# Kernel tuning notes

Hardware: AMD Instinct MI355X
Metric: run time of the kernel (lower is better)

Reference implementation:

```python
import jax, jax.numpy as jnp
import numpy as np

V, D, N, K, T, S = 128000, 128, 4, 4, 16, 5
EPS = 1e-10


def setup_inputs() -> dict:
    key = jax.random.key(0)
    k = jax.random.split(key, 5)
    return {
        "E": jax.random.normal(k[0], (V, D), jnp.float32) * 0.02,
        "bases": jax.random.normal(k[1], (K, N, D, D), jnp.float32) * (1.5 / np.sqrt(D)),
        "tension": jax.random.normal(k[2], (K, N, N), jnp.float32) * 0.1,
        "temperature": jnp.ones((K,), jnp.float32),
        "target_sim": jnp.full((K,), -1.0 / (N - 1), jnp.float32),
        "step_size": jnp.full((K,), 0.1, jnp.float32),
        "gate_logit": jnp.full((K,), -2.0, jnp.float32),
        "decay_base": jnp.asarray(0.8, jnp.float32),
        "sensitivity": jnp.asarray(1.0, jnp.float32),
        "noise": jax.random.normal(k[3], (T, K, S, N, D), jnp.float32),
        "tokens": jax.random.randint(k[4], (T,), 0, V),
    }


def reference(E, bases, tension, temperature, target_sim, step_size, gate_logit,
              decay_base, sensitivity, noise, tokens):
    mask = 1.0 - jnp.eye(N, dtype=E.dtype)
    temp = jnp.clip(jnp.abs(temperature), 0.01, None)
    # gauge interaction weights per foam: softmax over bubbles, self-interaction masked
    interaction = jax.nn.softmax(-tension / temp[:, None, None], axis=-1) * mask  # [K,N,N]
    step = jnp.clip(jnp.abs(step_size), 0.001, 0.5)           # [K]
    gate = jax.nn.sigmoid(gate_logit)                          # [K] noise gate
    sens = jnp.abs(sensitivity)

    def equilibrate(state0, B, inter, tgt, stp, g, nz):
        # state0 [N,D]; B [N,D,D] per-bubble bases; nz [S,N,D] pre-drawn perturbations
        def body(state, eps):
            expr = jnp.einsum('nd,nkd->nk', state, B)          # state_i @ basis_i.T
            expr_n = expr / (jnp.linalg.norm(expr, axis=-1, keepdims=True) + EPS)
            cos = expr_n @ expr_n.T                            # [N,N] pairwise cos-sim
            fmag = (cos - tgt) * inter                         # [N,N] force magnitudes
            diff = expr[:, None, :] - expr[None, :, :]         # [N,N,D]
            diff_n = diff / (jnp.linalg.norm(diff, axis=-1, keepdims=True) + EPS)
            f_shared = (fmag[..., None] * diff_n).sum(axis=1)  # [N,D]
            f_local = jnp.einsum('nk,nkd->nd', f_shared, B)    # back to local gauge
            scale = jnp.linalg.norm(state, axis=-1).mean() + EPS
            return state + stp * f_local + g * eps * scale * 0.01, None
        state, _ = jax.lax.scan(body, state0, nz)
        return state

    def foam_step(x, memory, B, inter, tgt, stp, g, nz):
        # x [D]; memory [N,D]
        mem_mean = memory.mean(axis=0)
        mem_norm = jnp.linalg.norm(mem_mean) + EPS
        x_norm = jnp.linalg.norm(x) + EPS
        nov = 1.0 - (x * mem_mean).sum() / (x_norm * mem_norm)
        novelty = jnp.where(mem_norm > 1e-8, nov, 1.0)
        decay = jax.nn.sigmoid(decay_base - sens * novelty)
        xm = x + decay * mem_mean
        eq = equilibrate(jnp.broadcast_to(xm, (N, D)), B, inter, tgt, stp, g, nz)
        rho = (eq.T @ eq) / ((eq * eq).sum() + EPS)            # trace-normalized density
        mem_new = decay * memory + (1.0 - decay) * eq
        return rho, mem_new

    xs_tok = E[tokens]                                         # [T,D]

    def token_step(memories, inp):
        x, nz_t = inp
        rhos, memories = jax.vmap(foam_step, in_axes=(None, 0, 0, 0, 0, 0, 0, 0))(
            x, memories, bases, interaction, target_sim, step, gate, nz_t)
        rho_mix = rhos.mean(axis=0)                            # [D,D]
        eig = jnp.clip(jnp.linalg.eigvalsh(rho_mix), 1e-12, None)
        eig = eig / eig.sum()
        logits = ((E @ rho_mix) * E).sum(axis=-1)              # born rule [V]
        logp = jax.nn.log_softmax(logits)
        probs = jnp.exp(logp)
        S_rho = -(eig * jnp.clip(jnp.log(eig), -100.0, None)).sum()
        H_tok = -(probs * jnp.clip(logp, -100.0, None)).sum()
        return memories, (probs, S_rho, H_tok, H_tok - S_rho)

    mem0 = jnp.zeros((K, N, D), E.dtype)
    _, (probs, S_rho, H_tok, F_tok) = jax.lax.scan(token_step, mem0, (xs_tok, noise))
    return probs, S_rho, H_tok, F_tok
```

## Files before the change

kernel.cpp:

```cpp
#include <hip/hip_runtime.h>
#include <math.h>

#define V_ 128000
#define D_ 128
#define N_ 4
#define K_ 4
#define T_ 16
#define S_ 5
#define EPSF 1e-10f

#define WS_G      0
#define WS_BEPS   262144
#define WS_BX     917504
#define WS_EQ2    950272
#define WS_EQBALL 954368
#define WS_GRAM   970752
#define WS_MM     974848
#define WS_BMM    975360
#define WS_INTER  977408
#define WS_WK     977472
#define WS_SRHO   977728
#define WS_LNZ    977744
#define WS_ZPART  977760
#define WS_EQF    977760
#define WS_HPART  1009760

typedef __attribute__((ext_vector_type(8))) short short8v;
typedef __attribute__((ext_vector_type(4))) float float4v;

__device__ __forceinline__ short bfb(float x) {
    unsigned u = __float_as_uint(x);
    u += 0x7fffu + ((u >> 16) & 1u);
    return (short)(u >> 16);
}

__device__ __forceinline__ void jpair(int x, int r, int& ox, bool& isp) {
    if (x == 15) { ox = r % 15; isp = true; return; }
    int s = x - r; s %= 15; if (s < 0) s += 15;
    if (s == 0) { ox = 15; isp = false; return; }
    int o = 2 * r - x; o %= 15; if (o < 0) o += 15;
    ox = o;
    isp = (s <= 7);
}

__device__ __forceinline__ void rotfast(float app, float aqq, float apq, float& c, float& s) {
    c = 1.f; s = 0.f;
    if (fabsf(apq) > 1e-20f) {
        float tau = (aqq - app) * 0.5f * __builtin_amdgcn_rcpf(apq);
        float sq1 = __builtin_amdgcn_sqrtf(1.f + tau * tau);
        float den = tau + ((tau >= 0.f) ? sq1 : -sq1);
        float tt = __builtin_amdgcn_rcpf(den);
        c = __builtin_amdgcn_rsqf(1.f + tt * tt);
        s = tt * c;
    }
}

__global__ __launch_bounds__(256)
void i2_prep(const float* __restrict__ bases, const float* __restrict__ E,
             const float* __restrict__ noise, const int* __restrict__ tokens,
             const float* __restrict__ tension, const float* __restrict__ temperature,
             float* __restrict__ ws)
{
    int tid = threadIdx.x;
    if (blockIdx.x == 64) {
        if (tid < 4) {
            int k = tid;
            float temp = fmaxf(fabsf(temperature[k]), 0.01f);
            for (int i = 0; i < 4; ++i) {
                float v[4]; float mx = -1e30f;
                for (int j = 0; j < 4; ++j) { v[j] = -tension[k*16 + i*4 + j] / temp; mx = fmaxf(mx, v[j]); }
                float se = 0.f;
                for (int j = 0; j < 4; ++j) { v[j] = expf(v[j] - mx); se += v[j]; }
                for (int j = 0; j < 4; ++j) ws[WS_INTER + k*16 + i*4 + j] = (i == j) ? 0.0f : v[j] / se;
            }
        }
        return;
    }
    int kn = blockIdx.x >> 2, q = blockIdx.x & 3;
    int k = kn >> 2, n = kn & 3;
    __shared__ __align__(16) float Blds[128 * 132];
    const float4* B4 = (const float4*)(bases + (size_t)kn * 16384);
    for (int idx = tid; idx < 4096; idx += 256) {
        int jrow = idx >> 5, c = idx & 31;
        float4 v = B4[jrow * 32 + c];
        *((float4*)&Blds[jrow * 132 + c * 4]) = v;
    }
    __syncthreads();
    int j1 = q * 32 + (tid >> 3);
    int l = tid & 7;
    float accg[16];
#pragma unroll
    for (int i = 0; i < 16; ++i) accg[i] = 0.f;
    for (int c = 0; c < 32; ++c) {
        float4 b1 = *((const float4*)&Blds[j1 * 132 + c * 4]);
#pragma unroll
        for (int i = 0; i < 16; ++i) {
            float4 b2 = *((const float4*)&Blds[(l + 8 * i) * 132 + c * 4]);
            accg[i] += b1.x * b2.x + b1.y * b2.y + b1.z * b2.z + b1.w * b2.w;
        }
    }
#pragma unroll
    for (int i = 0; i < 16; ++i) {
        int j2 = l + 8 * i;
        ws[WS_G + (((size_t)kn * 32 + (j2 >> 2)) * 128 + j1) * 4 + (j2 & 3)] = accg[i];
    }
    __shared__ __align__(16) float vecl[128];
    __shared__ float vred[2][128];
    int jv = tid & 127, ch = tid >> 7;
    for (int vi = q * 24; vi < q * 24 + 24; ++vi) {
        const float* src; int dstoff;
        if (vi < 16) {
            int tt = vi;
            src = E + (size_t)tokens[tt] * 128;
            dstoff = WS_BX + (tt * 4 + k) * 512 + n * 128;
        } else {
            int r2 = vi - 16; int tt = r2 / 5, s2 = r2 % 5;
            size_t off = (size_t)(((tt * 4 + k) * 5 + s2) * 4 + n) * 128;
            src = noise + off;
            dstoff = WS_BEPS + (int)off;
        }
        if (tid < 32) ((float4*)vecl)[tid] = ((const float4*)src)[tid];
        __syncthreads();
        float a2 = 0.f;
        for (int c = ch * 16; c < ch * 16 + 16; ++c) {
            float4 bv = *((const float4*)&Blds[jv * 132 + c * 4]);
            float4 xv = ((const float4*)vecl)[c];
            a2 += bv.x * xv.x + bv.y * xv.y + bv.z * xv.z + bv.w * xv.w;
        }
        vred[ch][jv] = a2;
        __syncthreads();
        if (tid < 128) ws[dstoff + tid] = vred[0][tid] + vred[1][tid];
        __syncthreads();
    }
}

__global__ __launch_bounds__(512, 2)
void kap_all(const float* __restrict__ E, const float* __restrict__ noise,
             const int* __restrict__ tokens, const float* __restrict__ bases,
             const float* __restrict__ target_sim, const float* __restrict__ step_size,
             const float* __restrict__ gate_logit, const float* __restrict__ decay_base,
             const float* __restrict__ sensitivity, float* __restrict__ ws)
{
    const int k = blockIdx.x;
    const int tid = threadIdx.x;
    const int n = tid >> 7;
    const int d = tid & 127;
    const int lane = tid & 63;
    const int wh = (tid >> 6) & 1;
    const int kn = k * 4 + n;

    __shared__ float xl[128];
    __shared__ __align__(16) float mlL[128];
    __shared__ __align__(16) float aL[4][128], exL[4][128];
    __shared__ float bmmL[4][128];
    __shared__ float interL[16];
    __shared__ float wredL[4][2][8];
    __shared__ float wredC[4][8];
    __shared__ float scal[1];

    float4 g[32];
    const float4* G4 = (const float4*)(ws + WS_G);
#pragma unroll
    for (int c = 0; c < 32; ++c) g[c] = G4[((size_t)kn * 32 + c) * 128 + d];

    if (tid < 16) interL[tid] = ws[WS_INTER + k * 16 + tid];
    if (tid < 128) mlL[tid] = 0.f;
    bmmL[n][d] = 0.f;

    const float tgt = target_sim[k];
    const float stp = fminf(fmaxf(fabsf(step_size[k]), 0.001f), 0.5f);
    const float gate = 1.0f / (1.0f + expf(-gate_logit[k]));
    const float dbase = decay_base[0];
    const float sens = fabsf(sensitivity[0]);
    __syncthreads();

#pragma unroll 1
    for (int t = 0; t < T_; ++t) {
        int tok = tokens[t];
        if (tid < 128) xl[tid] = E[(size_t)tok * 128 + tid];
        __syncthreads();

        if (tid < 64) {
            float x0 = xl[tid], x1 = xl[tid + 64];
            float m0 = mlL[tid], m1 = mlL[tid + 64];
            float vx = x0*x0 + x1*x1, vm = m0*m0 + m1*m1, vd = x0*m0 + x1*m1;
            for (int m = 32; m; m >>= 1) { vx += __shfl_xor(vx, m); vm += __shfl_xor(vm, m); vd += __shfl_xor(vd, m); }
            if (tid == 0) {
                float xnorm = sqrtf(vx) + EPSF, mnorm = sqrtf(vm) + EPSF;
                float nov = 1.0f - vd / (xnorm * mnorm);
                float novelty = (mnorm > 1e-8f) ? nov : 1.0f;
                scal[0] = 1.0f / (1.0f + expf(-(dbase - sens * novelty)));
            }
        }
        __syncthreads();
        const float dec = scal[0];

        float e0 = ws[WS_BX + (t*4 + k)*512 + n*128 + d] + dec * bmmL[n][d];
        float u  = xl[d] + dec * mlL[d];
        float ex = e0, a = 0.f, be = 0.f;
        exL[n][d] = ex;
        __syncthreads();

        for (int s = 0; s < 5; ++s) {
            int nz = (((t*4 + k)*5 + s)*4 + n) * 128 + d;
            float bepsv = ws[WS_BEPS + nz];
            float noisev = noise[nz];
            float em[4];
#pragma unroll
            for (int m = 0; m < 4; ++m) em[m] = exL[m][d];
            float r[7];
#pragma unroll
            for (int m = 0; m < 4; ++m) r[m] = ex * em[m];
            r[4] = u * u;
            r[5] = (e0 + be) * a;
            r[6] = a * (ex - e0 - be);
#pragma unroll
            for (int m2 = 32; m2; m2 >>= 1) {
#pragma unroll
                for (int q = 0; q < 7; ++q) r[q] += __shfl_xor(r[q], m2);
            }
            if (lane == 0) {
#pragma unroll
                for (int q = 0; q < 7; ++q) wredL[n][wh][q] = r[q];
            }
            __syncthreads();
            if (tid < 32) {
                int nn = tid >> 3, q = tid & 7;
                if (q < 7) wredC[nn][q] = wredL[nn][0][q] + wredL[nn][1][q];
            }
            __syncthreads();
            float ssum = 0.f;
#pragma unroll
            for (int m = 0; m < 4; ++m)
                ssum += sqrtf(fmaxf(wredC[m][4] + 2.f*wredC[m][5] + wredC[m][6], 0.f));
            float cn = gate * (0.25f * ssum + EPSF) * 0.01f;

            float Pnn = wredC[n][n];
            float enn = sqrtf(fmaxf(Pnn, 0.f)) + EPSF;
            float fsh = 0.f;
#pragma unroll
            for (int m = 0; m < 4; ++m) {
                float Pmm = wredC[m][m];
                float Pnm = wredC[n][m];
                float enm = sqrtf(fmaxf(Pmm, 0.f)) + EPSF;
                float cosnm = Pnm / (enn * enm);
                float fm = (cosnm - tgt) * interL[n * 4 + m];
                float dnn = sqrtf(fmaxf(Pnn - 2.f*Pnm + Pmm, 0.f)) + EPSF;
                float w = fm / dnn;
                fsh += w * (ex - em[m]);
            }
            a += stp * fsh;
            be += cn * bepsv;
            u += cn * noisev;
            aL[n][d] = a;
            __syncthreads();
            const float4* a4 = (const float4*)aL[n];
            float y = 0.f;
#pragma unroll
            for (int c = 0; c < 32; ++c) {
                float4 av = a4[c];
                y += g[c].x*av.x + g[c].y*av.y + g[c].z*av.z + g[c].w*av.w;
            }
            ex = e0 + y + be;
            exL[n][d] = ex;
            __syncthreads();
        }

        {
            const float* Bp = bases + (size_t)kn * 16384;
            float acc = 0.f;
#pragma unroll 8
            for (int j = 0; j < 128; ++j) acc += aL[n][j] * Bp[(size_t)j * 128 + d];
            float eq = u + acc;
            ws[WS_EQF + ((size_t)t * 16 + kn) * 128 + d] = eq;
            unsigned short* eqb = (unsigned short*)(ws + WS_EQBALL);
            int c2 = d >> 5, lg = (d >> 3) & 3, j8 = d & 7;
            eqb[t*2048 + (c2*64 + lg*16 + kn)*8 + j8] = (unsigned short)bfb(eq);
            float sq = eq * eq;
            for (int m = 32; m; m >>= 1) sq += __shfl_xor(sq, m);
            if (lane == 0) wredL[n][wh][7] = sq;
            exL[n][d] = eq;
            __syncthreads();
            if (tid < 4) {
                float s4 = 0.f;
#pragma unroll
                for (int m = 0; m < 4; ++m) s4 += wredL[m][0][7] + wredL[m][1][7];
                ws[WS_WK + t*16 + 4*k + tid] = 1.0f / (4.0f * (s4 + EPSF));
            }
            if (tid < 128) {
                float eqm = 0.25f * (exL[0][tid] + exL[1][tid] + exL[2][tid] + exL[3][tid]);
                mlL[tid] = dec * mlL[tid] + (1.f - dec) * eqm;
            }
            __syncthreads();
            const float4* Br = (const float4*)(bases + (size_t)kn * 16384 + (size_t)d * 128);
            const float4* mm4 = (const float4*)mlL;
            float bacc = 0.f;
#pragma unroll 8
            for (int c = 0; c < 32; ++c) {
                float4 bv = Br[c], mv = mm4[c];
                bacc += bv.x*mv.x + bv.y*mv.y + bv.z*mv.z + bv.w*mv.w;
            }
            bmmL[n][d] = bacc;
            __syncthreads();
        }
    }
}

__global__ __launch_bounds__(256)
void gramk(float* __restrict__ ws)
{
    int t = blockIdx.x, tid = threadIdx.x;
    int i = tid >> 4, j = tid & 15;
    const float4* ra = (const float4*)(ws + WS_EQF + ((size_t)t * 16 + i) * 128);
    const float4* rb = (const float4*)(ws + WS_EQF + ((size_t)t * 16 + j) * 128);
    float dp = 0.f;
#pragma unroll 8
    for (int c = 0; c < 32; ++c) {
        float4 a = ra[c], b2 = rb[c];
        dp += a.x * b2.x + a.y * b2.y + a.z * b2.z + a.w * b2.w;
    }
    ws[WS_GRAM + t * 256 + tid] = dp;
}

__global__ __launch_bounds__(256, 2)
void mega(const float* __restrict__ E, float* __restrict__ ws, float* __restrict__ out)
{
    int b = blockIdx.x, tid = threadIdx.x;
    if (b < 16) {
        if (tid >= 64) return;
        int tt = b;
        __shared__ float Am[16 * 20];
        __shared__ float cR[16], sR[16];
        int i0 = tid >> 2, j40 = (tid & 3) * 4;
        const float* G = ws + WS_GRAM + tt * 256;
        float wv4[4];
#pragma unroll
        for (int kk = 0; kk < 4; ++kk) {
            float ss = G[(4*kk+0)*17] + G[(4*kk+1)*17] + G[(4*kk+2)*17] + G[(4*kk+3)*17];
            wv4[kk] = 1.0f / (4.0f * (ss + EPSF));
        }
#pragma unroll
        for (int m = 0; m < 4; ++m) {
            int jjv = j40 + m;
            Am[i0 * 20 + jjv] = sqrtf(wv4[i0 >> 2] * wv4[jjv >> 2]) * G[i0 * 16 + jjv];
        }
        for (int sw = 0; sw < 6; ++sw) {
            for (int r = 0; r < 15; ++r) {
                if (tid < 8) {
                    int p, q;
                    if (tid == 0) { p = 15; q = r % 15; }
                    else { p = (r + tid) % 15; q = (r - tid + 15) % 15; }
                    float c, s;
                    rotfast(Am[p * 20 + p], Am[q * 20 + q], Am[p * 20 + q], c, s);
                    cR[p] = c; sR[p] = -s;
                    cR[q] = c; sR[q] = s;
                }
                int oi; bool ip; jpair(i0, r, oi, ip);
                float ci = cR[i0], siS = sR[i0];
                float nv[4];
#pragma unroll
                for (int m = 0; m < 4; ++m) {
                    int jjv = j40 + m;
                    int oj; bool jp2; jpair(jjv, r, oj, jp2);
                    float cj = cR[jjv], sjS = sR[jjv];
                    float a00 = Am[i0 * 20 + jjv], a01 = Am[i0 * 20 + oj];
                    float a10 = Am[oi * 20 + jjv], a11 = Am[oi * 20 + oj];
                    nv[m] = ci*cj*a00 + ci*sjS*a01 + siS*cj*a10 + siS*sjS*a11;
                }
#pragma unroll
                for (int m = 0; m < 4; ++m) Am[i0 * 20 + j40 + m] = nv[m];
            }
        }
        if (tid == 0) {
            float tot = 112.0f * 1e-12f;
            float lc[16];
            for (int a2 = 0; a2 < 16; ++a2) { lc[a2] = fmaxf(Am[a2 * 20 + a2], 1e-12f); tot += lc[a2]; }
            float S = 0.f;
            for (int a2 = 0; a2 < 16; ++a2) { float pp = lc[a2] / tot; S -= pp * fmaxf(logf(pp), -100.f); }
            float p0 = 1e-12f / tot;
            S -= 112.f * p0 * fmaxf(logf(p0), -100.f);
            out[(size_t)T_ * V_ + tt] = S;
            ws[WS_SRHO + tt] = S;
        }
        return;
    }
    int b2 = b - 16;
    int pass = b2 / 500;
    int bb = b2 - pass * 500;
    int tok0 = pass * 4;
    int lane = tid & 63, wv = tid >> 6;
    const short8v* eqB = (const short8v*)(ws + WS_EQBALL);
    short8v bfr[4][4];
#pragma unroll
    for (int tk = 0; tk < 4; ++tk)
#pragma unroll
        for (int c2 = 0; c2 < 4; ++c2) bfr[tk][c2] = eqB[(tok0 + tk) * 256 + c2 * 64 + lane];
    float wk[4], zl[4];
#pragma unroll
    for (int tk = 0; tk < 4; ++tk) {
        wk[tk] = ws[WS_WK + (tok0 + tk) * 16 + (lane & 15)];
        zl[tk] = 0.f;
    }
    int tilebase = (bb * 4 + wv) * 64;
#pragma unroll
    for (int it = 0; it < 4; ++it) {
        int rowB = tilebase + it * 16;
        const float* Erow = E + (size_t)(rowB + (lane & 15)) * 128 + ((lane >> 4) * 8);
        float4v acc[4];
#pragma unroll
        for (int tk = 0; tk < 4; ++tk) acc[tk] = (float4v){0.f, 0.f, 0.f, 0.f};
#pragma unroll
        for (int c2 = 0; c2 < 4; ++c2) {
            float4 e0 = *((const float4*)(Erow + c2 * 32));
            float4 e1 = *((const float4*)(Erow + c2 * 32 + 4));
            short8v a;
            a[0] = bfb(e0.x); a[1] = bfb(e0.y); a[2] = bfb(e0.z); a[3] = bfb(e0.w);
            a[4] = bfb(e1.x); a[5] = bfb(e1.y); a[6] = bfb(e1.z); a[7] = bfb(e1.w);
#pragma unroll
            for (int tk = 0; tk < 4; ++tk)
                acc[tk] = __builtin_amdgcn_mfma_f32_16x16x32_bf16(a, bfr[tk][c2], acc[tk], 0, 0, 0);
        }
#pragma unroll
        for (int tk = 0; tk < 4; ++tk) {
            float l0 = wk[tk] * acc[tk][0] * acc[tk][0];
            float l1 = wk[tk] * acc[tk][1] * acc[tk][1];
            float l2 = wk[tk] * acc[tk][2] * acc[tk][2];
            float l3 = wk[tk] * acc[tk][3] * acc[tk][3];
#pragma unroll
            for (int m = 1; m <= 8; m <<= 1) {
                l0 += __shfl_xor(l0, m); l1 += __shfl_xor(l1, m);
                l2 += __shfl_xor(l2, m); l3 += __shfl_xor(l3, m);
            }
            if ((lane & 15) == 0) {
                float4 st; st.x = l0; st.y = l1; st.z = l2; st.w = l3;
                *((float4*)(out + (size_t)(tok0 + tk) * V_ + rowB + (lane >> 4) * 4)) = st;
                zl[tk] += __expf(l0) + __expf(l1) + __expf(l2) + __expf(l3);
            }
        }
    }
#pragma unroll
    for (int tk = 0; tk < 4; ++tk) {
        float z = zl[tk];
        z += __shfl_xor(z, 16); z += __shfl_xor(z, 32);
        if (lane == 0) ws[WS_ZPART + (tok0 + tk) * 2000 + bb * 4 + wv] = z;
    }
}

__global__ __launch_bounds__(256)
void zk(float* __restrict__ ws)
{
    int b = blockIdx.x, tid = threadIdx.x;
    double s = 0.0;
    for (int i = tid; i < 2000; i += 256) s += (double)ws[WS_ZPART + b * 2000 + i];
    for (int m = 32; m; m >>= 1) s += __shfl_xor(s, m);
    __shared__ double sr[4];
    if ((tid & 63) == 0) sr[tid >> 6] = s;
    __syncthreads();
    if (tid == 0) ws[WS_LNZ + b] = (float)log(sr[0] + sr[1] + sr[2] + sr[3]);
}

__global__ __launch_bounds__(256)
void fin1(float* __restrict__ ws, float* __restrict__ out)
{
    int b = blockIdx.x, tid = threadIdx.x;
    int tt = b / 125, blk = b - tt * 125;
    int v = blk * 1024 + tid * 4;
    float lnZ = ws[WS_LNZ + tt];
    float* po = out + (size_t)tt * V_ + v;
    float4 l4 = *((const float4*)po);
    float lp0 = l4.x - lnZ, lp1 = l4.y - lnZ, lp2 = l4.z - lnZ, lp3 = l4.w - lnZ;
    float p0 = __expf(lp0), p1 = __expf(lp1), p2 = __expf(lp2), p3 = __expf(lp3);
    float4 st; st.x = p0; st.y = p1; st.z = p2; st.w = p3;
    *((float4*)po) = st;
    float hp = p0 * fmaxf(lp0, -100.f) + p1 * fmaxf(lp1, -100.f)
             + p2 * fmaxf(lp2, -100.f) + p3 * fmaxf(lp3, -100.f);
    for (int m = 32; m; m >>= 1) hp += __shfl_xor(hp, m);
    __shared__ float hr[4];
    if ((tid & 63) == 0) hr[tid >> 6] = hp;
    __syncthreads();
    if (tid == 0) ws[WS_HPART + tt * 125 + blk] = hr[0] + hr[1] + hr[2] + hr[3];
}

__global__ __launch_bounds__(128)
void f2_final(float* __restrict__ ws, float* __restrict__ out)
{
    int t = blockIdx.x, tid = threadIdx.x;
    float s = (tid < 125) ? ws[WS_HPART + t * 125 + tid] : 0.f;
    for (int m = 32; m; m >>= 1) s += __shfl_xor(s, m);
    __shared__ float sr[2];
    if ((tid & 63) == 0) sr[tid >> 6] = s;
    __syncthreads();
    if (tid == 0) {
        float H = -(sr[0] + sr[1]);
        float S = ws[WS_SRHO + t];
        out[(size_t)T_ * V_ + T_ + t] = H;
        out[(size_t)T_ * V_ + 2 * T_ + t] = H - S;
    }
}

extern "C" void kernel_launch(void* const* d_in, const int* in_sizes, int n_in,
                              void* d_out, int out_size, void* d_ws, size_t ws_size,
                              hipStream_t stream)
{
    (void)in_sizes; (void)n_in; (void)out_size; (void)ws_size;
    const float* E           = (const float*)d_in[0];
    const float* bases       = (const float*)d_in[1];
    const float* tension     = (const float*)d_in[2];
    const float* temperature = (const float*)d_in[3];
    const float* target_sim  = (const float*)d_in[4];
    const float* step_size   = (const float*)d_in[5];
    const float* gate_logit  = (const float*)d_in[6];
    const float* decay_base  = (const float*)d_in[7];
    const float* sensitivity = (const float*)d_in[8];
    const float* noise       = (const float*)d_in[9];
    const int*   tokens      = (const int*)d_in[10];
    float* out = (float*)d_out;
    float* ws  = (float*)d_ws;

    i2_prep<<<65, 256, 0, stream>>>(bases, E, noise, tokens, tension, temperature, ws);
    kap_all<<<4, 512, 0, stream>>>(E, noise, tokens, bases, target_sim, step_size,
                                   gate_logit, decay_base, sensitivity, ws);
    gramk<<<16, 256, 0, stream>>>(ws);
    mega<<<2016, 256, 0, stream>>>(E, ws, out);
    zk<<<16, 256, 0, stream>>>(ws);
    fin1<<<T_ * 125, 256, 0, stream>>>(ws, out);
    f2_final<<<T_, 128, 0, stream>>>(ws, out);
}
```

Measured before the change: 646.2 us.

## Shrink recurrence kernel to one wave per bubble, fuse gram, widen logits tile

The sequential recurrence kernel now runs 256 threads with each wave owning one bubble and two dims per lane. This lets reductions finish within a wave, removes a cross-wave LDS stage and several barriers per step, and prefetches noise, tokens and memory projections into registers. The separate gram kernel is folded into the mega kernel's first blocks, reusing the freed noise-projection buffer for the equilibrium output. The logits GEMM now processes 8 tokens per block instead of 4, halving E reads at the cost of more registers.

```diff
diff --git a/kernel.cpp b/kernel.cpp
--- a/kernel.cpp
+++ b/kernel.cpp
@@ -12,17 +12,12 @@
 #define WS_G      0
 #define WS_BEPS   262144
 #define WS_BX     917504
-#define WS_EQ2    950272
 #define WS_EQBALL 954368
-#define WS_GRAM   970752
-#define WS_MM     974848
-#define WS_BMM    975360
 #define WS_INTER  977408
 #define WS_WK     977472
 #define WS_SRHO   977728
 #define WS_LNZ    977744
 #define WS_ZPART  977760
-#define WS_EQF    977760
 #define WS_HPART  1009760
 
 typedef __attribute__((ext_vector_type(8))) short short8v;
@@ -134,7 +129,7 @@
     }
 }
 
-__global__ __launch_bounds__(512, 2)
+__global__ __launch_bounds__(256, 1)
 void kap_all(const float* __restrict__ E, const float* __restrict__ noise,
              const int* __restrict__ tokens, const float* __restrict__ bases,
              const float* __restrict__ target_sim, const float* __restrict__ step_size,
@@ -143,183 +138,172 @@
 {
     const int k = blockIdx.x;
     const int tid = threadIdx.x;
-    const int n = tid >> 7;
-    const int d = tid & 127;
+    const int n = tid >> 6;
     const int lane = tid & 63;
-    const int wh = (tid >> 6) & 1;
+    const int d0 = lane, d1 = lane + 64;
     const int kn = k * 4 + n;
 
     __shared__ float xl[128];
     __shared__ __align__(16) float mlL[128];
     __shared__ __align__(16) float aL[4][128], exL[4][128];
-    __shared__ float bmmL[4][128];
     __shared__ float interL[16];
-    __shared__ float wredL[4][2][8];
-    __shared__ float wredC[4][8];
-    __shared__ float scal[1];
-
-    float4 g[32];
+    __shared__ float diagP[4], sP[4], sq7[4];
+
+    float4 g0[32], g1[32];
     const float4* G4 = (const float4*)(ws + WS_G);
 #pragma unroll
-    for (int c = 0; c < 32; ++c) g[c] = G4[((size_t)kn * 32 + c) * 128 + d];
+    for (int c = 0; c < 32; ++c) {
+        g0[c] = G4[((size_t)kn * 32 + c) * 128 + d0];
+        g1[c] = G4[((size_t)kn * 32 + c) * 128 + d1];
+    }
 
     if (tid < 16) interL[tid] = ws[WS_INTER + k * 16 + tid];
     if (tid < 128) mlL[tid] = 0.f;
-    bmmL[n][d] = 0.f;
 
     const float tgt = target_sim[k];
     const float stp = fminf(fmaxf(fabsf(step_size[k]), 0.001f), 0.5f);
     const float gate = 1.0f / (1.0f + expf(-gate_logit[k]));
     const float dbase = decay_base[0];
     const float sens = fabsf(sensitivity[0]);
+
+    float xr = (tid < 128) ? E[(size_t)tokens[0] * 128 + tid] : 0.f;
+    float bmm0 = 0.f, bmm1 = 0.f;
     __syncthreads();
+    float w_inter[4];
+#pragma unroll
+    for (int m = 0; m < 4; ++m) w_inter[m] = interL[n * 4 + m];
 
 #pragma unroll 1
     for (int t = 0; t < T_; ++t) {
-        int tok = tokens[t];
-        if (tid < 128) xl[tid] = E[(size_t)tok * 128 + tid];
+        if (tid < 128) xl[tid] = xr;
         __syncthreads();
-
-        if (tid < 64) {
-            float x0 = xl[tid], x1 = xl[tid + 64];
-            float m0 = mlL[tid], m1 = mlL[tid + 64];
-            float vx = x0*x0 + x1*x1, vm = m0*m0 + m1*m1, vd = x0*m0 + x1*m1;
-            for (int m = 32; m; m >>= 1) { vx += __shfl_xor(vx, m); vm += __shfl_xor(vm, m); vd += __shfl_xor(vd, m); }
-            if (tid == 0) {
-                float xnorm = sqrtf(vx) + EPSF, mnorm = sqrtf(vm) + EPSF;
-                float nov = 1.0f - vd / (xnorm * mnorm);
-                float novelty = (mnorm > 1e-8f) ? nov : 1.0f;
-                scal[0] = 1.0f / (1.0f + expf(-(dbase - sens * novelty)));
-            }
-        }
+        if (t + 1 < T_ && tid < 128) xr = E[(size_t)tokens[t + 1] * 128 + tid];
+
+        float bep0[5], bep1[5], no0[5], no1[5];
+#pragma unroll
+        for (int s = 0; s < 5; ++s) {
+            int nz = (((t * 4 + k) * 5 + s) * 4 + n) * 128;
+            bep0[s] = ws[WS_BEPS + nz + d0]; bep1[s] = ws[WS_BEPS + nz + d1];
+            no0[s] = noise[nz + d0];         no1[s] = noise[nz + d1];
+        }
+        float bx0 = ws[WS_BX + (t * 4 + k) * 512 + n * 128 + d0];
+        float bx1 = ws[WS_BX + (t * 4 + k) * 512 + n * 128 + d1];
+
+        float x0 = xl[d0], x1 = xl[d1], m0 = mlL[d0], m1 = mlL[d1];
+        float vx = x0 * x0 + x1 * x1, vm = m0 * m0 + m1 * m1, vd = x0 * m0 + x1 * m1;
+        for (int m = 32; m; m >>= 1) { vx += __shfl_xor(vx, m); vm += __shfl_xor(vm, m); vd += __shfl_xor(vd, m); }
+        float xnorm = sqrtf(vx) + EPSF, mnorm = sqrtf(vm) + EPSF;
+        float nov = 1.0f - vd / (xnorm * mnorm);
+        float novelty = (mnorm > 1e-8f) ? nov : 1.0f;
+        const float dec = 1.0f / (1.0f + expf(-(dbase - sens * novelty)));
+
+        float e00 = bx0 + dec * bmm0, e01 = bx1 + dec * bmm1;
+        float u0 = x0 + dec * m0, u1 = x1 + dec * m1;
+        float ex0 = e00, ex1 = e01, a0 = 0.f, a1 = 0.f, be0 = 0.f, be1 = 0.f;
+        exL[n][d0] = ex0; exL[n][d1] = ex1;
         __syncthreads();
-        const float dec = scal[0];
-
-        float e0 = ws[WS_BX + (t*4 + k)*512 + n*128 + d] + dec * bmmL[n][d];
-        float u  = xl[d] + dec * mlL[d];
-        float ex = e0, a = 0.f, be = 0.f;
-        exL[n][d] = ex;
-        __syncthreads();
 
         for (int s = 0; s < 5; ++s) {
-            int nz = (((t*4 + k)*5 + s)*4 + n) * 128 + d;
-            float bepsv = ws[WS_BEPS + nz];
-            float noisev = noise[nz];
-            float em[4];
-#pragma unroll
-            for (int m = 0; m < 4; ++m) em[m] = exL[m][d];
+            float em0[4], em1[4];
+#pragma unroll
+            for (int m = 0; m < 4; ++m) { em0[m] = exL[m][d0]; em1[m] = exL[m][d1]; }
             float r[7];
 #pragma unroll
-            for (int m = 0; m < 4; ++m) r[m] = ex * em[m];
-            r[4] = u * u;
-            r[5] = (e0 + be) * a;
-            r[6] = a * (ex - e0 - be);
+            for (int m = 0; m < 4; ++m) r[m] = ex0 * em0[m] + ex1 * em1[m];
+            r[4] = u0 * u0 + u1 * u1;
+            r[5] = (e00 + be0) * a0 + (e01 + be1) * a1;
+            r[6] = a0 * (ex0 - e00 - be0) + a1 * (ex1 - e01 - be1);
 #pragma unroll
             for (int m2 = 32; m2; m2 >>= 1) {
 #pragma unroll
                 for (int q = 0; q < 7; ++q) r[q] += __shfl_xor(r[q], m2);
             }
-            if (lane == 0) {
-#pragma unroll
-                for (int q = 0; q < 7; ++q) wredL[n][wh][q] = r[q];
-            }
+            float sn = sqrtf(fmaxf(r[4] + 2.f * r[5] + r[6], 0.f));
+            if (lane == 0) { diagP[n] = r[n]; sP[n] = sn; }
             __syncthreads();
-            if (tid < 32) {
-                int nn = tid >> 3, q = tid & 7;
-                if (q < 7) wredC[nn][q] = wredL[nn][0][q] + wredL[nn][1][q];
-            }
-            __syncthreads();
-            float ssum = 0.f;
-#pragma unroll
-            for (int m = 0; m < 4; ++m)
-                ssum += sqrtf(fmaxf(wredC[m][4] + 2.f*wredC[m][5] + wredC[m][6], 0.f));
+            float ssum = ((sP[0] + sP[1]) + sP[2]) + sP[3];
             float cn = gate * (0.25f * ssum + EPSF) * 0.01f;
 
-            float Pnn = wredC[n][n];
+            float Pnn = r[n];
             float enn = sqrtf(fmaxf(Pnn, 0.f)) + EPSF;
-            float fsh = 0.f;
+            float fsh0 = 0.f, fsh1 = 0.f;
 #pragma unroll
             for (int m = 0; m < 4; ++m) {
-                float Pmm = wredC[m][m];
-                float Pnm = wredC[n][m];
+                float Pmm = diagP[m];
+                float Pnm = r[m];
                 float enm = sqrtf(fmaxf(Pmm, 0.f)) + EPSF;
                 float cosnm = Pnm / (enn * enm);
-                float fm = (cosnm - tgt) * interL[n * 4 + m];
-                float dnn = sqrtf(fmaxf(Pnn - 2.f*Pnm + Pmm, 0.f)) + EPSF;
+                float fm = (cosnm - tgt) * w_inter[m];
+                float dnn = sqrtf(fmaxf(Pnn - 2.f * Pnm + Pmm, 0.f)) + EPSF;
                 float w = fm / dnn;
-                fsh += w * (ex - em[m]);
-            }
-            a += stp * fsh;
-            be += cn * bepsv;
-            u += cn * noisev;
-            aL[n][d] = a;
-            __syncthreads();
+                fsh0 += w * (ex0 - em0[m]);
+                fsh1 += w * (ex1 - em1[m]);
+            }
+            a0 += stp * fsh0; a1 += stp * fsh1;
+            be0 += cn * bep0[s]; be1 += cn * bep1[s];
+            u0 += cn * no0[s];   u1 += cn * no1[s];
+            aL[n][d0] = a0; aL[n][d1] = a1;
             const float4* a4 = (const float4*)aL[n];
-            float y = 0.f;
+            float y0 = 0.f, y1 = 0.f;
 #pragma unroll
             for (int c = 0; c < 32; ++c) {
                 float4 av = a4[c];
-                y += g[c].x*av.x + g[c].y*av.y + g[c].z*av.z + g[c].w*av.w;
-            }
-            ex = e0 + y + be;
-            exL[n][d] = ex;
+                y0 += g0[c].x * av.x + g0[c].y * av.y + g0[c].z * av.z + g0[c].w * av.w;
+                y1 += g1[c].x * av.x + g1[c].y * av.y + g1[c].z * av.z + g1[c].w * av.w;
+            }
+            ex0 = e00 + y0 + be0; ex1 = e01 + y1 + be1;
+            exL[n][d0] = ex0; exL[n][d1] = ex1;
             __syncthreads();
         }
 
         {
             const float* Bp = bases + (size_t)kn * 16384;
-            float acc = 0.f;
+            float acc0 = 0.f, acc1 = 0.f;
 #pragma unroll 8
-            for (int j = 0; j < 128; ++j) acc += aL[n][j] * Bp[(size_t)j * 128 + d];
-            float eq = u + acc;
-            ws[WS_EQF + ((size_t)t * 16 + kn) * 128 + d] = eq;
+            for (int j = 0; j < 128; ++j) {
+                float aj = aL[n][j];
+                acc0 += aj * Bp[(size_t)j * 128 + d0];
+                acc1 += aj * Bp[(size_t)j * 128 + d1];
+            }
+            float eq0 = u0 + acc0, eq1 = u1 + acc1;
+            int eqfbase = WS_BEPS + t * 10240 + k * 2560 + n * 128;
+            ws[eqfbase + d0] = eq0; ws[eqfbase + d1] = eq1;
             unsigned short* eqb = (unsigned short*)(ws + WS_EQBALL);
-            int c2 = d >> 5, lg = (d >> 3) & 3, j8 = d & 7;
-            eqb[t*2048 + (c2*64 + lg*16 + kn)*8 + j8] = (unsigned short)bfb(eq);
-            float sq = eq * eq;
+            {
+                int c2 = d0 >> 5, lg = (d0 >> 3) & 3, j8 = d0 & 7;
+                eqb[t * 2048 + (c2 * 64 + lg * 16 + kn) * 8 + j8] = (unsigned short)bfb(eq0);
+            }
+            {
+                int c2 = d1 >> 5, lg = (d1 >> 3) & 3, j8 = d1 & 7;
+                eqb[t * 2048 + (c2 * 64 + lg * 16 + kn) * 8 + j8] = (unsigned short)bfb(eq1);
+            }
+            float sq = eq0 * eq0 + eq1 * eq1;
             for (int m = 32; m; m >>= 1) sq += __shfl_xor(sq, m);
-            if (lane == 0) wredL[n][wh][7] = sq;
-            exL[n][d] = eq;
+            if (lane == 0) sq7[n] = sq;
+            exL[n][d0] = eq0; exL[n][d1] = eq1;
             __syncthreads();
             if (tid < 4) {
-                float s4 = 0.f;
-#pragma unroll
-                for (int m = 0; m < 4; ++m) s4 += wredL[m][0][7] + wredL[m][1][7];
-                ws[WS_WK + t*16 + 4*k + tid] = 1.0f / (4.0f * (s4 + EPSF));
+                float s4 = sq7[0] + sq7[1] + sq7[2] + sq7[3];
+                ws[WS_WK + t * 16 + 4 * k + tid] = 1.0f / (4.0f * (s4 + EPSF));
             }
             if (tid < 128) {
                 float eqm = 0.25f * (exL[0][tid] + exL[1][tid] + exL[2][tid] + exL[3][tid]);
                 mlL[tid] = dec * mlL[tid] + (1.f - dec) * eqm;
             }
             __syncthreads();
-            const float4* Br = (const float4*)(bases + (size_t)kn * 16384 + (size_t)d * 128);
+            const float4* Br0 = (const float4*)(bases + (size_t)kn * 16384 + (size_t)d0 * 128);
+            const float4* Br1 = (const float4*)(bases + (size_t)kn * 16384 + (size_t)d1 * 128);
             const float4* mm4 = (const float4*)mlL;
-            float bacc = 0.f;
+            bmm0 = 0.f; bmm1 = 0.f;
 #pragma unroll 8
             for (int c = 0; c < 32; ++c) {
-                float4 bv = Br[c], mv = mm4[c];
-                bacc += bv.x*mv.x + bv.y*mv.y + bv.z*mv.z + bv.w*mv.w;
-            }
-            bmmL[n][d] = bacc;
-            __syncthreads();
-        }
-    }
-}
-
-__global__ __launch_bounds__(256)
-void gramk(float* __restrict__ ws)
-{
-    int t = blockIdx.x, tid = threadIdx.x;
-    int i = tid >> 4, j = tid & 15;
-    const float4* ra = (const float4*)(ws + WS_EQF + ((size_t)t * 16 + i) * 128);
-    const float4* rb = (const float4*)(ws + WS_EQF + ((size_t)t * 16 + j) * 128);
-    float dp = 0.f;
-#pragma unroll 8
-    for (int c = 0; c < 32; ++c) {
-        float4 a = ra[c], b2 = rb[c];
-        dp += a.x * b2.x + a.y * b2.y + a.z * b2.z + a.w * b2.w;
-    }
-    ws[WS_GRAM + t * 256 + tid] = dp;
+                float4 mv = mm4[c];
+                float4 v0 = Br0[c], v1 = Br1[c];
+                bmm0 += v0.x * mv.x + v0.y * mv.y + v0.z * mv.z + v0.w * mv.w;
+                bmm1 += v1.x * mv.x + v1.y * mv.y + v1.z * mv.z + v1.w * mv.w;
+            }
+        }
+    }
 }
 
 __global__ __launch_bounds__(256, 2)
@@ -327,12 +311,26 @@
 {
     int b = blockIdx.x, tid = threadIdx.x;
     if (b < 16) {
-        if (tid >= 64) return;
         int tt = b;
+        __shared__ float Gsh[256];
         __shared__ float Am[16 * 20];
         __shared__ float cR[16], sR[16];
+        {
+            int i = tid >> 4, j = tid & 15;
+            const float4* ra = (const float4*)(ws + WS_BEPS + tt * 10240 + (i >> 2) * 2560 + (i & 3) * 128);
+            const float4* rb = (const float4*)(ws + WS_BEPS + tt * 10240 + (j >> 2) * 2560 + (j & 3) * 128);
+            float dp = 0.f;
+#pragma unroll 8
+            for (int c = 0; c < 32; ++c) {
+                float4 a = ra[c], b2 = rb[c];
+                dp += a.x * b2.x + a.y * b2.y + a.z * b2.z + a.w * b2.w;
+            }
+            Gsh[tid] = dp;
+        }
+        __syncthreads();
+        if (tid >= 64) return;
+        const float* G = Gsh;
         int i0 = tid >> 2, j40 = (tid & 3) * 4;
-        const float* G = ws + WS_GRAM + tt * 256;
         float wv4[4];
 #pragma unroll
         for (int kk = 0; kk < 4; ++kk) {
@@ -387,17 +385,17 @@
     int b2 = b - 16;
     int pass = b2 / 500;
     int bb = b2 - pass * 500;
-    int tok0 = pass * 4;
+    int tok0 = pass * 8;
     int lane = tid & 63, wv = tid >> 6;
     const short8v* eqB = (const short8v*)(ws + WS_EQBALL);
-    short8v bfr[4][4];
-#pragma unroll
-    for (int tk = 0; tk < 4; ++tk)
+    short8v bfr[8][4];
+#pragma unroll
+    for (int tk = 0; tk < 8; ++tk)
 #pragma unroll
         for (int c2 = 0; c2 < 4; ++c2) bfr[tk][c2] = eqB[(tok0 + tk) * 256 + c2 * 64 + lane];
-    float wk[4], zl[4];
-#pragma unroll
-    for (int tk = 0; tk < 4; ++tk) {
+    float wk[8], zl[8];
+#pragma unroll
+    for (int tk = 0; tk < 8; ++tk) {
         wk[tk] = ws[WS_WK + (tok0 + tk) * 16 + (lane & 15)];
         zl[tk] = 0.f;
     }
@@ -406,9 +404,9 @@
     for (int it = 0; it < 4; ++it) {
         int rowB = tilebase + it * 16;
         const float* Erow = E + (size_t)(rowB + (lane & 15)) * 128 + ((lane >> 4) * 8);
-        float4v acc[4];
-#pragma unroll
-        for (int tk = 0; tk < 4; ++tk) acc[tk] = (float4v){0.f, 0.f, 0.f, 0.f};
+        float4v acc[8];
+#pragma unroll
+        for (int tk = 0; tk < 8; ++tk) acc[tk] = (float4v){0.f, 0.f, 0.f, 0.f};
 #pragma unroll
         for (int c2 = 0; c2 < 4; ++c2) {
             float4 e0 = *((const float4*)(Erow + c2 * 32));
@@ -417,11 +415,11 @@
             a[0] = bfb(e0.x); a[1] = bfb(e0.y); a[2] = bfb(e0.z); a[3] = bfb(e0.w);
             a[4] = bfb(e1.x); a[5] = bfb(e1.y); a[6] = bfb(e1.z); a[7] = bfb(e1.w);
 #pragma unroll
-            for (int tk = 0; tk < 4; ++tk)
+            for (int tk = 0; tk < 8; ++tk)
                 acc[tk] = __builtin_amdgcn_mfma_f32_16x16x32_bf16(a, bfr[tk][c2], acc[tk], 0, 0, 0);
         }
 #pragma unroll
-        for (int tk = 0; tk < 4; ++tk) {
+        for (int tk = 0; tk < 8; ++tk) {
             float l0 = wk[tk] * acc[tk][0] * acc[tk][0];
             float l1 = wk[tk] * acc[tk][1] * acc[tk][1];
             float l2 = wk[tk] * acc[tk][2] * acc[tk][2];
@@ -439,7 +437,7 @@
         }
     }
 #pragma unroll
-    for (int tk = 0; tk < 4; ++tk) {
+    for (int tk = 0; tk < 8; ++tk) {
         float z = zl[tk];
         z += __shfl_xor(z, 16); z += __shfl_xor(z, 32);
         if (lane == 0) ws[WS_ZPART + (tok0 + tk) * 2000 + bb * 4 + wv] = z;
@@ -518,10 +516,9 @@
     float* ws  = (float*)d_ws;
 
     i2_prep<<<65, 256, 0, stream>>>(bases, E, noise, tokens, tension, temperature, ws);
-    kap_all<<<4, 512, 0, stream>>>(E, noise, tokens, bases, target_sim, step_size,
+    kap_all<<<4, 256, 0, stream>>>(E, noise, tokens, bases, target_sim, step_size,
                                    gate_logit, decay_base, sensitivity, ws);
-    gramk<<<16, 256, 0, stream>>>(ws);
-    mega<<<2016, 256, 0, stream>>>(E, ws, out);
+    mega<<<1016, 256, 0, stream>>>(E, ws, out);
     zk<<<16, 256, 0, stream>>>(ws);
     fin1<<<T_ * 125, 256, 0, stream>>>(ws, out);
     f2_final<<<T_, 128, 0, stream>>>(ws, out);
```

After: 805.6 us. 1.25x slower.
